# Kernel tuning notes

Hardware: AMD Instinct MI355X
Metric: run time of the kernel (lower is better)

The kernel has to match this reference:

```python
import jax, jax.numpy as jnp
import numpy as np

NEG_SLOPE = 0.2  # PyG GATConv default leaky_relu slope


def _add_self_loops(edge_index, num_nodes):
    loop = jnp.arange(num_nodes, dtype=edge_index.dtype)
    return jnp.concatenate([edge_index, jnp.stack([loop, loop])], axis=1)


def _gat_conv(x, edge_index, W, a_src, a_dst, b, heads, out_c):
    # x: [N, Fin]; W: [Fin, heads*out_c]; a_src/a_dst: [heads, out_c]; b: [heads*out_c]
    N = x.shape[0]
    h = (x @ W).reshape(N, heads, out_c)                       # [N,H,C]
    src, dst = edge_index[0], edge_index[1]
    alpha_src = jnp.einsum('nhc,hc->nh', h, a_src)             # [N,H]
    alpha_dst = jnp.einsum('nhc,hc->nh', h, a_dst)             # [N,H]
    e = jax.nn.leaky_relu(alpha_src[src] + alpha_dst[dst], NEG_SLOPE)  # [E,H]
    # segment softmax over edges grouped by destination node
    m = jax.ops.segment_max(e, dst, num_segments=N)
    m = jnp.where(jnp.isfinite(m), m, jnp.zeros_like(m))
    ex = jnp.exp(e - m[dst])
    denom = jax.ops.segment_sum(ex, dst, num_segments=N)
    alpha = ex / (denom[dst] + 1e-16)                          # [E,H]
    out = jax.ops.segment_sum(h[src] * alpha[:, :, None], dst, num_segments=N)
    return out.reshape(N, heads * out_c) + b


def setup_inputs() -> dict:
    key = jax.random.key(0)
    ks = jax.random.split(key, 16)
    N, E, FIN, HID, HEADS, OUT = 50000, 800000, 128, 32, 4, 64
    x = jax.random.normal(ks[0], (N, FIN), dtype=jnp.float32)
    edge_index = jax.random.randint(ks[1], (2, E), 0, N, dtype=jnp.int64)
    s = 0.1
    inp = {
        'x': x, 'edge_index': edge_index,
        'W0': jax.random.normal(ks[2], (FIN, HEADS * HID), jnp.float32) * s,
        'asrc0': jax.random.normal(ks[3], (HEADS, HID), jnp.float32) * s,
        'adst0': jax.random.normal(ks[4], (HEADS, HID), jnp.float32) * s,
        'b0': jnp.zeros((HEADS * HID,), jnp.float32),
        'W1': jax.random.normal(ks[5], (HEADS * HID, HEADS * HID), jnp.float32) * s,
        'asrc1': jax.random.normal(ks[6], (HEADS, HID), jnp.float32) * s,
        'adst1': jax.random.normal(ks[7], (HEADS, HID), jnp.float32) * s,
        'b1': jnp.zeros((HEADS * HID,), jnp.float32),
        'W2': jax.random.normal(ks[8], (HEADS * HID, OUT), jnp.float32) * s,
        'asrc2': jax.random.normal(ks[9], (1, OUT), jnp.float32) * s,
        'adst2': jax.random.normal(ks[10], (1, OUT), jnp.float32) * s,
        'b2': jnp.zeros((OUT,), jnp.float32),
    }
    return inp


def reference(x, edge_index, W0, asrc0, adst0, b0, W1, asrc1, adst1, b1, W2, asrc2, adst2, b2):
    # Dropout is identity in eval mode.
    N = x.shape[0]
    ei = _add_self_loops(edge_index, N)
    h = _gat_conv(x, ei, W0, asrc0, adst0, b0, heads=4, out_c=32)
    h = jax.nn.relu(h)
    h = _gat_conv(h, ei, W1, asrc1, adst1, b1, heads=4, out_c=32)
    h = jax.nn.relu(h)
    out = _gat_conv(h, ei, W2, asrc2, adst2, b2, heads=1, out_c=64)
    return out
```

## Files before the change

### kernel.cpp

```cpp
#include <hip/hip_runtime.h>


#define NEG_SLOPE 0.2f

typedef _Float16 f16;
typedef f16 f16x8 __attribute__((ext_vector_type(8)));
typedef f16 f16x4 __attribute__((ext_vector_type(4)));
typedef f16 f16x2 __attribute__((ext_vector_type(2)));
typedef float f32x4 __attribute__((ext_vector_type(4)));

__device__ __forceinline__ float lrelu(float v) { return v > 0.f ? v : NEG_SLOPE * v; }


__global__ void fill_zero_kernel(int* __restrict__ p, int n) {
    int i = blockIdx.x * blockDim.x + threadIdx.x;
    if (i < n) p[i] = 0;
}

__global__ __launch_bounds__(256) void bucket_count_kernel(const int* __restrict__ dst, int E,
                                                           int* __restrict__ bcount) {
    __shared__ int lh[256];
    lh[threadIdx.x] = 0;
    __syncthreads();
    int stride = gridDim.x * 256 * 4;
    for (int i = (blockIdx.x * 256 + threadIdx.x) * 4; i < E; i += stride) {
        int4 d = *(const int4*)&dst[i];
        atomicAdd(&lh[d.x >> 8], 1);
        atomicAdd(&lh[d.y >> 8], 1);
        atomicAdd(&lh[d.z >> 8], 1);
        atomicAdd(&lh[d.w >> 8], 1);
    }
    __syncthreads();
    int v = lh[threadIdx.x];
    if (v > 0) atomicAdd(&bcount[threadIdx.x], v);
}

__global__ __launch_bounds__(256) void bucket_scan_kernel(const int* __restrict__ bcount, int NBK,
                                                          int* __restrict__ bbase,
                                                          int* __restrict__ bcursor,
                                                          int* __restrict__ offsets, int N) {
    int t = threadIdx.x;
    int own = (t < NBK) ? bcount[t] : 0;
    int v = own;
    int lane = t & 63, wid = t >> 6;
#pragma unroll
    for (int off = 1; off < 64; off <<= 1) {
        int u = __shfl_up(v, off);
        if (lane >= off) v += u;
    }
    __shared__ int ws[4];
    if (lane == 63) ws[wid] = v;
    __syncthreads();
    int add = 0;
    for (int w = 0; w < wid; ++w) add += ws[w];
    v += add;
    int exc = v - own;
    if (t < NBK) {
        bbase[t] = exc;
        bcursor[t] = exc;
    }
    if (t == 255) {
        bbase[NBK] = v;
        offsets[N] = v;
    }
}

#define SC_TILE 4096
__global__ __launch_bounds__(256) void bucket_scatter_kernel(const int* __restrict__ src,
                                                             const int* __restrict__ dst, int E,
                                                             int* __restrict__ bcursor,
                                                             unsigned int* __restrict__ staging) {
    __shared__ int lh[256];
    __shared__ int lcur[256];
    int tid = threadIdx.x;
    lh[tid] = 0;
    __syncthreads();
    int base = blockIdx.x * SC_TILE + tid * 16;
    int sv[16], dv[16];
    bool act = base < E;
    if (act) {
#pragma unroll
        for (int q = 0; q < 4; ++q) {
            *(int4*)&sv[q * 4] = *(const int4*)&src[base + q * 4];
            *(int4*)&dv[q * 4] = *(const int4*)&dst[base + q * 4];
        }
#pragma unroll
        for (int j = 0; j < 16; ++j) atomicAdd(&lh[dv[j] >> 8], 1);
    }
    __syncthreads();
    int c = lh[tid];
    if (c > 0) lcur[tid] = atomicAdd(&bcursor[tid], c);
    __syncthreads();
    if (act) {
#pragma unroll
        for (int j = 0; j < 16; ++j) {
            int b = dv[j] >> 8;
            int pos = atomicAdd(&lcur[b], 1);
            staging[pos] = (unsigned int)sv[j] | ((unsigned int)(dv[j] & 255) << 16);
        }
    }
}

#define SORT_CAP 8192
__global__ __launch_bounds__(256) void bucket_sort_kernel(const unsigned int* __restrict__ staging,
                                                          const int* __restrict__ bbase,
                                                          int* __restrict__ offsets,
                                                          int* __restrict__ ssrc, int N) {
    __shared__ unsigned int buf[SORT_CAP];
    __shared__ unsigned short sout[SORT_CAP];
    __shared__ int lh[256];
    __shared__ int ws[4];
    int b = blockIdx.x;
    int tid = threadIdx.x;
    int s = bbase[b], e = bbase[b + 1];
    int cnt = e - s;
    lh[tid] = 0;
    __syncthreads();
    bool fits = cnt <= SORT_CAP;
    if (fits) {
        for (int i = tid; i < cnt; i += 256) {
            unsigned int rec = staging[s + i];
            buf[i] = rec;
            atomicAdd(&lh[rec >> 16], 1);
        }
    } else {
        for (int i = tid; i < cnt; i += 256) atomicAdd(&lh[staging[s + i] >> 16], 1);
    }
    __syncthreads();
    int own = lh[tid];
    int v = own;
    int lane = tid & 63, wid = tid >> 6;
#pragma unroll
    for (int off = 1; off < 64; off <<= 1) {
        int u = __shfl_up(v, off);
        if (lane >= off) v += u;
    }
    if (lane == 63) ws[wid] = v;
    __syncthreads();
    int add = 0;
    for (int w = 0; w < wid; ++w) add += ws[w];
    int exc = v + add - own;
    int dstn = (b << 8) + tid;
    if (dstn < N) offsets[dstn] = s + exc;
    __syncthreads();
    lh[tid] = exc;
    __syncthreads();
    if (fits) {
        for (int i = tid; i < cnt; i += 256) {
            unsigned int rec = buf[i];
            int r = atomicAdd(&lh[rec >> 16], 1);
            sout[r] = (unsigned short)(rec & 0xFFFFu);
        }
        __syncthreads();
        for (int i = tid; i < cnt; i += 256) ssrc[s + i] = (int)sout[i];
    } else {
        for (int i = tid; i < cnt; i += 256) {
            unsigned int rec = staging[s + i];
            int r = atomicAdd(&lh[rec >> 16], 1);
            ssrc[s + r] = (int)(rec & 0xFFFFu);
        }
    }
}


__global__ void split_x_kernel(const float* __restrict__ x, f16* __restrict__ xh,
                               f16* __restrict__ xl, int total4) {
    int i = blockIdx.x * blockDim.x + threadIdx.x;
    if (i >= total4) return;
    float4 v = *(const float4*)&x[(size_t)i * 4];
    float vv[4] = {v.x, v.y, v.z, v.w};
    f16x4 h, l;
#pragma unroll
    for (int j = 0; j < 4; ++j) {
        f16 hj = (f16)vv[j];
        h[j] = hj;
        l[j] = (f16)(vv[j] - (float)hj);
    }
    *(f16x4*)&xh[(size_t)i * 4] = h;
    *(f16x4*)&xl[(size_t)i * 4] = l;
}

__global__ void split_w_kernel(const float* __restrict__ W0, const float* __restrict__ W1,
                               const float* __restrict__ W2, f16* __restrict__ w0h,
                               f16* __restrict__ w0l, f16* __restrict__ w1h,
                               f16* __restrict__ w1l, f16* __restrict__ w2h,
                               f16* __restrict__ w2l) {
    int idx = blockIdx.x * 256 + threadIdx.x;
    if (idx < 16384) {
        int k = idx >> 7, c = idx & 127;
        float v = W0[k * 128 + c];
        f16 h = (f16)v;
        w0h[c * 128 + k] = h;
        w0l[c * 128 + k] = (f16)(v - (float)h);
    } else if (idx < 32768) {
        int t = idx - 16384;
        int k = t >> 7, c = t & 127;
        float v = W1[k * 128 + c];
        f16 h = (f16)v;
        w1h[c * 128 + k] = h;
        w1l[c * 128 + k] = (f16)(v - (float)h);
    } else if (idx < 40960) {
        int t = idx - 32768;
        int k = t >> 6, c = t & 63;
        float v = W2[k * 64 + c];
        f16 h = (f16)v;
        w2h[c * 128 + k] = h;
        w2l[c * 128 + k] = (f16)(v - (float)h);
    }
}

template <int FOUT>
__global__ __launch_bounds__(256) void gemm_mfma_kernel(
    const f16* __restrict__ Ah, const f16* __restrict__ Al, const f16* __restrict__ Bh,
    const f16* __restrict__ Bl, f16* __restrict__ H16, int N) {
    constexpr int CT = FOUT / 16;
    __shared__ f16 lw[2][FOUT][72];
    int tid = threadIdx.x;
    int w = tid >> 6, lane = tid & 63;
    int quad = lane >> 4, m = lane & 15;
    int row0 = blockIdx.x * 64 + w * 16;
    int arow = row0 + m;
    if (arow >= N) arow = N - 1;
    const f16* aph = &Ah[(size_t)arow * 128 + quad * 8];
    const f16* apl = &Al[(size_t)arow * 128 + quad * 8];

    f32x4 acc[CT];
#pragma unroll
    for (int t = 0; t < CT; ++t) acc[t] = (f32x4){0.f, 0.f, 0.f, 0.f};

    for (int kh = 0; kh < 2; ++kh) {
        __syncthreads();
        for (int f = tid; f < FOUT * 8; f += 256) {
            int col = f >> 3, ch = f & 7;
            *(f16x8*)&lw[0][col][ch * 8] = *(const f16x8*)&Bh[(size_t)col * 128 + kh * 64 + ch * 8];
            *(f16x8*)&lw[1][col][ch * 8] = *(const f16x8*)&Bl[(size_t)col * 128 + kh * 64 + ch * 8];
        }
        __syncthreads();
#pragma unroll
        for (int kc = 0; kc < 2; ++kc) {
            f16x8 fah = *(const f16x8*)&aph[kh * 64 + kc * 32];
            f16x8 fal = *(const f16x8*)&apl[kh * 64 + kc * 32];
#pragma unroll
            for (int t = 0; t < CT; ++t) {
                f16x8 fbh = *(const f16x8*)&lw[0][t * 16 + m][kc * 32 + quad * 8];
                f16x8 fbl = *(const f16x8*)&lw[1][t * 16 + m][kc * 32 + quad * 8];
                acc[t] = __builtin_amdgcn_mfma_f32_16x16x32_f16(fah, fbh, acc[t], 0, 0, 0);
                acc[t] = __builtin_amdgcn_mfma_f32_16x16x32_f16(fal, fbh, acc[t], 0, 0, 0);
                acc[t] = __builtin_amdgcn_mfma_f32_16x16x32_f16(fah, fbl, acc[t], 0, 0, 0);
            }
        }
    }
#pragma unroll
    for (int r = 0; r < 4; ++r) {
        int row = row0 + quad * 4 + r;
        if (row < N) {
#pragma unroll
            for (int t = 0; t < CT; ++t)
                H16[(size_t)row * FOUT + t * 16 + m] = (f16)acc[t][r];
        }
    }
}

template <int H_, int C>
__global__ void alpha_kernel(const f16* __restrict__ h16, const float* __restrict__ a_src,
                             const float* __restrict__ a_dst, float* __restrict__ asrc,
                             float* __restrict__ adst, int N) {
    int idx = blockIdx.x * blockDim.x + threadIdx.x;
    if (idx >= N * H_) return;
    int n = idx / H_, h = idx % H_;
    const f16* hp = &h16[(size_t)n * H_ * C + h * C];
    const float* as = &a_src[h * C];
    const float* ad = &a_dst[h * C];
    float s1 = 0.f, s2 = 0.f;
#pragma unroll
    for (int c8 = 0; c8 < C / 8; ++c8) {
        f16x8 v = *(const f16x8*)&hp[c8 * 8];
#pragma unroll
        for (int j = 0; j < 8; ++j) {
            float vv = (float)v[j];
            s1 += vv * as[c8 * 8 + j];
            s2 += vv * ad[c8 * 8 + j];
        }
    }
    asrc[idx] = s1;
    adst[idx] = s2;
}

template <int H_, int C, bool RELU, bool SPLIT_OUT>
__global__ __launch_bounds__(256) void aggr_kernel(
    const f16* __restrict__ h16, const float* __restrict__ asrc,
    const float* __restrict__ adst, const float* __restrict__ bias,
    const int* __restrict__ offsets, const int* __restrict__ ssrc, float* __restrict__ outf,
    f16* __restrict__ outh, f16* __restrict__ outl, int N) {
    constexpr int FOUT = H_ * C;
    constexpr int PER = FOUT / 64;
    int wid = threadIdx.x >> 6;
    int lane = threadIdx.x & 63;
    int n = blockIdx.x * 4 + wid;
    if (n >= N) return;
    int c0 = lane * PER;
    int head = c0 / C;

    float adst_h = adst[n * H_ + head];
    float m = lrelu(asrc[n * H_ + head] + adst_h);
    float D = 1.f;
    float S0, S1 = 0.f;
    if (PER == 2) {
        f16x2 hv = *(const f16x2*)&h16[(size_t)n * FOUT + c0];
        S0 = (float)hv[0];
        S1 = (float)hv[1];
    } else {
        S0 = (float)h16[(size_t)n * FOUT + c0];
    }

    int k = offsets[n];
    const int e1 = offsets[n + 1];

    for (; k + 4 <= e1; k += 4) {
        int s0 = ssrc[k], s1 = ssrc[k + 1], s2 = ssrc[k + 2], s3 = ssrc[k + 3];
        f16x2 h0, h1, h2, h3;
        float g0 = 0.f, g1 = 0.f, g2 = 0.f, g3 = 0.f;
        if (PER == 2) {
            h0 = *(const f16x2*)&h16[(size_t)s0 * FOUT + c0];
            h1 = *(const f16x2*)&h16[(size_t)s1 * FOUT + c0];
            h2 = *(const f16x2*)&h16[(size_t)s2 * FOUT + c0];
            h3 = *(const f16x2*)&h16[(size_t)s3 * FOUT + c0];
        } else {
            g0 = (float)h16[(size_t)s0 * FOUT + c0];
            g1 = (float)h16[(size_t)s1 * FOUT + c0];
            g2 = (float)h16[(size_t)s2 * FOUT + c0];
            g3 = (float)h16[(size_t)s3 * FOUT + c0];
        }
        float E0 = lrelu(asrc[s0 * H_ + head] + adst_h);
        float E1 = lrelu(asrc[s1 * H_ + head] + adst_h);
        float E2 = lrelu(asrc[s2 * H_ + head] + adst_h);
        float E3 = lrelu(asrc[s3 * H_ + head] + adst_h);
        float mn = fmaxf(m, fmaxf(fmaxf(E0, E1), fmaxf(E2, E3)));
        float sc = __expf(m - mn);
        m = mn;
        D *= sc;
        S0 *= sc;
        if (PER == 2) S1 *= sc;
        float x0 = __expf(E0 - m), x1 = __expf(E1 - m);
        float x2 = __expf(E2 - m), x3 = __expf(E3 - m);
        D += (x0 + x1) + (x2 + x3);
        if (PER == 2) {
            S0 += x0 * (float)h0[0] + x1 * (float)h1[0] + x2 * (float)h2[0] + x3 * (float)h3[0];
            S1 += x0 * (float)h0[1] + x1 * (float)h1[1] + x2 * (float)h2[1] + x3 * (float)h3[1];
        } else {
            S0 += x0 * g0 + x1 * g1 + x2 * g2 + x3 * g3;
        }
    }
    for (; k < e1; ++k) {
        int s = ssrc[k];
        f16x2 hv;
        float gv = 0.f;
        if (PER == 2) {
            hv = *(const f16x2*)&h16[(size_t)s * FOUT + c0];
        } else {
            gv = (float)h16[(size_t)s * FOUT + c0];
        }
        float E = lrelu(asrc[s * H_ + head] + adst_h);
        float mn = fmaxf(m, E);
        float sc = __expf(m - mn);
        m = mn;
        D *= sc;
        S0 *= sc;
        if (PER == 2) S1 *= sc;
        float ex = __expf(E - m);
        D += ex;
        if (PER == 2) {
            S0 += ex * (float)hv[0];
            S1 += ex * (float)hv[1];
        } else {
            S0 += ex * gv;
        }
    }

    float inv = 1.f / (D + 1e-16f);
    float v0 = S0 * inv + bias[c0];
    if (RELU) v0 = fmaxf(v0, 0.f);
    if (SPLIT_OUT) {
        float v1 = S1 * inv + bias[c0 + 1];
        if (RELU) v1 = fmaxf(v1, 0.f);
        f16 h0 = (f16)v0, h1 = (f16)v1;
        f16x2 hh = {h0, h1};
        f16x2 ll = {(f16)(v0 - (float)h0), (f16)(v1 - (float)h1)};
        *(f16x2*)&outh[(size_t)n * FOUT + c0] = hh;
        *(f16x2*)&outl[(size_t)n * FOUT + c0] = ll;
    } else if (PER == 2) {
        float v1 = S1 * inv + bias[c0 + 1];
        if (RELU) v1 = fmaxf(v1, 0.f);
        *(float2*)&outf[(size_t)n * FOUT + c0] = make_float2(v0, v1);
    } else {
        outf[(size_t)n * FOUT + c0] = v0;
    }
}

extern "C" void kernel_launch(void* const* d_in, const int* in_sizes, int n_in,
                              void* d_out, int out_size, void* d_ws, size_t ws_size,
                              hipStream_t stream) {
    const float* x = (const float*)d_in[0];
    const int* ei = (const int*)d_in[1];
    const float* W0 = (const float*)d_in[2];
    const float* as0 = (const float*)d_in[3];
    const float* ad0 = (const float*)d_in[4];
    const float* b0 = (const float*)d_in[5];
    const float* W1 = (const float*)d_in[6];
    const float* as1 = (const float*)d_in[7];
    const float* ad1 = (const float*)d_in[8];
    const float* b1 = (const float*)d_in[9];
    const float* W2 = (const float*)d_in[10];
    const float* as2 = (const float*)d_in[11];
    const float* ad2 = (const float*)d_in[12];
    const float* b2 = (const float*)d_in[13];

    const int N = in_sizes[0] / 128;
    const int E = in_sizes[1] / 2;
    const int NBK = (N + 255) >> 8;

    float* aS = (float*)d_ws;
    float* aD = aS + (size_t)N * 4;
    f16* h16 = (f16*)(aD + (size_t)N * 4);
    f16* xh = h16 + (size_t)N * 128;
    f16* xl = xh + (size_t)N * 128;
    f16* w0h = xl + (size_t)N * 128;
    f16* w0l = w0h + 16384;
    f16* w1h = w0l + 16384;
    f16* w1l = w1h + 16384;
    f16* w2h = w1l + 16384;
    f16* w2l = w2h + 8192;
    int* offsets = (int*)(w2l + 8192);
    int* ssrc = offsets + N + 1;
    unsigned int* staging = (unsigned int*)(ssrc + E);
    int* bcount = (int*)(staging + E);
    int* bbase = bcount + NBK;
    int* bcursor = bbase + NBK + 1;

    fill_zero_kernel<<<1, 256, 0, stream>>>(bcount, NBK);
    bucket_count_kernel<<<196, 256, 0, stream>>>(ei + E, E, bcount);
    bucket_scan_kernel<<<1, 256, 0, stream>>>(bcount, NBK, bbase, bcursor, offsets, N);
    bucket_scatter_kernel<<<(E + SC_TILE - 1) / SC_TILE, 256, 0, stream>>>(ei, ei + E, E, bcursor,
                                                                           staging);
    bucket_sort_kernel<<<NBK, 256, 0, stream>>>(staging, bbase, offsets, ssrc, N);

    split_x_kernel<<<(N * 32 + 255) / 256, 256, 0, stream>>>(x, xh, xl, N * 32);
    split_w_kernel<<<160, 256, 0, stream>>>(W0, W1, W2, w0h, w0l, w1h, w1l, w2h, w2l);

    const int gGemm = (N + 63) / 64;
    const int gAggr = (N + 3) / 4;

    gemm_mfma_kernel<128><<<gGemm, 256, 0, stream>>>(xh, xl, w0h, w0l, h16, N);
    alpha_kernel<4, 32><<<(N * 4 + 255) / 256, 256, 0, stream>>>(h16, as0, ad0, aS, aD, N);
    aggr_kernel<4, 32, true, true><<<gAggr, 256, 0, stream>>>(h16, aS, aD, b0, offsets, ssrc,
                                                              nullptr, xh, xl, N);
    gemm_mfma_kernel<128><<<gGemm, 256, 0, stream>>>(xh, xl, w1h, w1l, h16, N);
    alpha_kernel<4, 32><<<(N * 4 + 255) / 256, 256, 0, stream>>>(h16, as1, ad1, aS, aD, N);
    aggr_kernel<4, 32, true, true><<<gAggr, 256, 0, stream>>>(h16, aS, aD, b1, offsets, ssrc,
                                                              nullptr, xh, xl, N);
    gemm_mfma_kernel<64><<<gGemm, 256, 0, stream>>>(xh, xl, w2h, w2l, h16, N);
    alpha_kernel<1, 64><<<(N + 255) / 256, 256, 0, stream>>>(h16, as2, ad2, aS, aD, N);
    aggr_kernel<1, 64, false, false><<<gAggr, 256, 0, stream>>>(h16, aS, aD, b2, offsets, ssrc,
                                                                (float*)d_out, nullptr, nullptr, N);
}
```

Before: 322.6 us.

## Precompute per-edge softmax weights using the self-loop logit as stabilizer

Adds an edge-weight kernel that computes exp(e - e_self) per edge and head, using each destination's self-loop logit in place of the running maximum. The aggregation kernel then reads these precomputed weights with vector loads instead of gathering attention scores and doing online-max rescaling and exp for every lane. To make this possible, the sort kernel now packs the destination index into the upper 16 bits of each sorted source entry and drops its shared-memory staging, which gives up coalesced writes. In exchange it adds an extra E×heads float buffer written and read per layer, adds a launch per layer, and risks exp overflow if an edge logit far exceeds the self-loop logit.

```diff
diff --git a/kernel.cpp b/kernel.cpp
--- a/kernel.cpp
+++ b/kernel.cpp
@@ -101,13 +101,10 @@
     }
 }
 
-#define SORT_CAP 8192
 __global__ __launch_bounds__(256) void bucket_sort_kernel(const unsigned int* __restrict__ staging,
                                                           const int* __restrict__ bbase,
                                                           int* __restrict__ offsets,
                                                           int* __restrict__ ssrc, int N) {
-    __shared__ unsigned int buf[SORT_CAP];
-    __shared__ unsigned short sout[SORT_CAP];
     __shared__ int lh[256];
     __shared__ int ws[4];
     int b = blockIdx.x;
@@ -116,16 +113,7 @@
     int cnt = e - s;
     lh[tid] = 0;
     __syncthreads();
-    bool fits = cnt <= SORT_CAP;
-    if (fits) {
-        for (int i = tid; i < cnt; i += 256) {
-            unsigned int rec = staging[s + i];
-            buf[i] = rec;
-            atomicAdd(&lh[rec >> 16], 1);
-        }
-    } else {
-        for (int i = tid; i < cnt; i += 256) atomicAdd(&lh[staging[s + i] >> 16], 1);
-    }
+    for (int i = tid; i < cnt; i += 256) atomicAdd(&lh[staging[s + i] >> 16], 1);
     __syncthreads();
     int own = lh[tid];
     int v = own;
@@ -145,20 +133,12 @@
     __syncthreads();
     lh[tid] = exc;
     __syncthreads();
-    if (fits) {
-        for (int i = tid; i < cnt; i += 256) {
-            unsigned int rec = buf[i];
-            int r = atomicAdd(&lh[rec >> 16], 1);
-            sout[r] = (unsigned short)(rec & 0xFFFFu);
-        }
-        __syncthreads();
-        for (int i = tid; i < cnt; i += 256) ssrc[s + i] = (int)sout[i];
-    } else {
-        for (int i = tid; i < cnt; i += 256) {
-            unsigned int rec = staging[s + i];
-            int r = atomicAdd(&lh[rec >> 16], 1);
-            ssrc[s + r] = (int)(rec & 0xFFFFu);
-        }
+    for (int i = tid; i < cnt; i += 256) {
+        unsigned int rec = staging[s + i];
+        int dlow = rec >> 16;
+        int r = atomicAdd(&lh[dlow], 1);
+        unsigned int full = (rec & 0xFFFFu) | ((unsigned int)((b << 8) | dlow) << 16);
+        ssrc[s + r] = (int)full;
     }
 }
 
@@ -286,12 +266,32 @@
     adst[idx] = s2;
 }
 
+template <int H_>
+__global__ void edgew_kernel(const int* __restrict__ ssrc, const float* __restrict__ asrc,
+                             const float* __restrict__ adst, float* __restrict__ w, int E) {
+    int k = blockIdx.x * 256 + threadIdx.x;
+    if (k >= E) return;
+    unsigned int rec = (unsigned int)ssrc[k];
+    int s = rec & 0xFFFFu, d = rec >> 16;
+    if (H_ == 4) {
+        float4 a_s = *(const float4*)&asrc[s * 4];
+        float4 a_dd = *(const float4*)&adst[d * 4];
+        float4 a_sd = *(const float4*)&asrc[d * 4];
+        w[0 * E + k] = __expf(lrelu(a_s.x + a_dd.x) - lrelu(a_sd.x + a_dd.x));
+        w[1 * E + k] = __expf(lrelu(a_s.y + a_dd.y) - lrelu(a_sd.y + a_dd.y));
+        w[2 * E + k] = __expf(lrelu(a_s.z + a_dd.z) - lrelu(a_sd.z + a_dd.z));
+        w[3 * E + k] = __expf(lrelu(a_s.w + a_dd.w) - lrelu(a_sd.w + a_dd.w));
+    } else {
+        w[k] = __expf(lrelu(asrc[s] + adst[d]) - lrelu(asrc[d] + adst[d]));
+    }
+}
+
 template <int H_, int C, bool RELU, bool SPLIT_OUT>
 __global__ __launch_bounds__(256) void aggr_kernel(
-    const f16* __restrict__ h16, const float* __restrict__ asrc,
-    const float* __restrict__ adst, const float* __restrict__ bias,
-    const int* __restrict__ offsets, const int* __restrict__ ssrc, float* __restrict__ outf,
-    f16* __restrict__ outh, f16* __restrict__ outl, int N) {
+    const f16* __restrict__ h16, const float* __restrict__ wedge,
+    const float* __restrict__ bias, const int* __restrict__ offsets,
+    const int* __restrict__ ssrc, float* __restrict__ outf, f16* __restrict__ outh,
+    f16* __restrict__ outl, int N, int E) {
     constexpr int FOUT = H_ * C;
     constexpr int PER = FOUT / 64;
     int wid = threadIdx.x >> 6;
@@ -300,80 +300,66 @@
     if (n >= N) return;
     int c0 = lane * PER;
     int head = c0 / C;
-
-    float adst_h = adst[n * H_ + head];
-    float m = lrelu(asrc[n * H_ + head] + adst_h);
+    const float* wb = wedge + head * E;
+
     float D = 1.f;
     float S0, S1 = 0.f;
     if (PER == 2) {
-        f16x2 hv = *(const f16x2*)&h16[(size_t)n * FOUT + c0];
+        f16x2 hv = *(const f16x2*)&h16[n * FOUT + c0];
         S0 = (float)hv[0];
         S1 = (float)hv[1];
     } else {
-        S0 = (float)h16[(size_t)n * FOUT + c0];
+        S0 = (float)h16[n * FOUT + c0];
     }
 
     int k = offsets[n];
     const int e1 = offsets[n + 1];
 
+    for (; k < e1 && (k & 3); ++k) {
+        int s = ssrc[k] & 0xFFFF;
+        float w = wb[k];
+        D += w;
+        if (PER == 2) {
+            f16x2 hv = *(const f16x2*)&h16[s * FOUT + c0];
+            S0 += w * (float)hv[0];
+            S1 += w * (float)hv[1];
+        } else {
+            S0 += w * (float)h16[s * FOUT + c0];
+        }
+    }
     for (; k + 4 <= e1; k += 4) {
-        int s0 = ssrc[k], s1 = ssrc[k + 1], s2 = ssrc[k + 2], s3 = ssrc[k + 3];
-        f16x2 h0, h1, h2, h3;
-        float g0 = 0.f, g1 = 0.f, g2 = 0.f, g3 = 0.f;
+        int4 pk = *(const int4*)&ssrc[k];
+        float4 wv = *(const float4*)&wb[k];
+        int s0 = pk.x & 0xFFFF, s1 = pk.y & 0xFFFF, s2 = pk.z & 0xFFFF, s3 = pk.w & 0xFFFF;
         if (PER == 2) {
-            h0 = *(const f16x2*)&h16[(size_t)s0 * FOUT + c0];
-            h1 = *(const f16x2*)&h16[(size_t)s1 * FOUT + c0];
-            h2 = *(const f16x2*)&h16[(size_t)s2 * FOUT + c0];
-            h3 = *(const f16x2*)&h16[(size_t)s3 * FOUT + c0];
+            f16x2 h0 = *(const f16x2*)&h16[s0 * FOUT + c0];
+            f16x2 h1 = *(const f16x2*)&h16[s1 * FOUT + c0];
+            f16x2 h2 = *(const f16x2*)&h16[s2 * FOUT + c0];
+            f16x2 h3 = *(const f16x2*)&h16[s3 * FOUT + c0];
+            D += (wv.x + wv.y) + (wv.z + wv.w);
+            S0 += wv.x * (float)h0[0] + wv.y * (float)h1[0] + wv.z * (float)h2[0] +
+                  wv.w * (float)h3[0];
+            S1 += wv.x * (float)h0[1] + wv.y * (float)h1[1] + wv.z * (float)h2[1] +
+                  wv.w * (float)h3[1];
         } else {
-            g0 = (float)h16[(size_t)s0 * FOUT + c0];
-            g1 = (float)h16[(size_t)s1 * FOUT + c0];
-            g2 = (float)h16[(size_t)s2 * FOUT + c0];
-            g3 = (float)h16[(size_t)s3 * FOUT + c0];
-        }
-        float E0 = lrelu(asrc[s0 * H_ + head] + adst_h);
-        float E1 = lrelu(asrc[s1 * H_ + head] + adst_h);
-        float E2 = lrelu(asrc[s2 * H_ + head] + adst_h);
-        float E3 = lrelu(asrc[s3 * H_ + head] + adst_h);
-        float mn = fmaxf(m, fmaxf(fmaxf(E0, E1), fmaxf(E2, E3)));
-        float sc = __expf(m - mn);
-        m = mn;
-        D *= sc;
-        S0 *= sc;
-        if (PER == 2) S1 *= sc;
-        float x0 = __expf(E0 - m), x1 = __expf(E1 - m);
-        float x2 = __expf(E2 - m), x3 = __expf(E3 - m);
-        D += (x0 + x1) + (x2 + x3);
+            float g0 = (float)h16[s0 * FOUT + c0];
+            float g1 = (float)h16[s1 * FOUT + c0];
+            float g2 = (float)h16[s2 * FOUT + c0];
+            float g3 = (float)h16[s3 * FOUT + c0];
+            D += (wv.x + wv.y) + (wv.z + wv.w);
+            S0 += wv.x * g0 + wv.y * g1 + wv.z * g2 + wv.w * g3;
+        }
+    }
+    for (; k < e1; ++k) {
+        int s = ssrc[k] & 0xFFFF;
+        float w = wb[k];
+        D += w;
         if (PER == 2) {
-            S0 += x0 * (float)h0[0] + x1 * (float)h1[0] + x2 * (float)h2[0] + x3 * (float)h3[0];
-            S1 += x0 * (float)h0[1] + x1 * (float)h1[1] + x2 * (float)h2[1] + x3 * (float)h3[1];
+            f16x2 hv = *(const f16x2*)&h16[s * FOUT + c0];
+            S0 += w * (float)hv[0];
+            S1 += w * (float)hv[1];
         } else {
-            S0 += x0 * g0 + x1 * g1 + x2 * g2 + x3 * g3;
-        }
-    }
-    for (; k < e1; ++k) {
-        int s = ssrc[k];
-        f16x2 hv;
-        float gv = 0.f;
-        if (PER == 2) {
-            hv = *(const f16x2*)&h16[(size_t)s * FOUT + c0];
-        } else {
-            gv = (float)h16[(size_t)s * FOUT + c0];
-        }
-        float E = lrelu(asrc[s * H_ + head] + adst_h);
-        float mn = fmaxf(m, E);
-        float sc = __expf(m - mn);
-        m = mn;
-        D *= sc;
-        S0 *= sc;
-        if (PER == 2) S1 *= sc;
-        float ex = __expf(E - m);
-        D += ex;
-        if (PER == 2) {
-            S0 += ex * (float)hv[0];
-            S1 += ex * (float)hv[1];
-        } else {
-            S0 += ex * gv;
+            S0 += w * (float)h16[s * FOUT + c0];
         }
     }
 
@@ -386,14 +372,14 @@
         f16 h0 = (f16)v0, h1 = (f16)v1;
         f16x2 hh = {h0, h1};
         f16x2 ll = {(f16)(v0 - (float)h0), (f16)(v1 - (float)h1)};
-        *(f16x2*)&outh[(size_t)n * FOUT + c0] = hh;
-        *(f16x2*)&outl[(size_t)n * FOUT + c0] = ll;
+        *(f16x2*)&outh[n * FOUT + c0] = hh;
+        *(f16x2*)&outl[n * FOUT + c0] = ll;
     } else if (PER == 2) {
         float v1 = S1 * inv + bias[c0 + 1];
         if (RELU) v1 = fmaxf(v1, 0.f);
-        *(float2*)&outf[(size_t)n * FOUT + c0] = make_float2(v0, v1);
+        *(float2*)&outf[n * FOUT + c0] = make_float2(v0, v1);
     } else {
-        outf[(size_t)n * FOUT + c0] = v0;
+        outf[n * FOUT + c0] = v0;
     }
 }
 
@@ -433,7 +419,8 @@
     int* offsets = (int*)(w2l + 8192);
     int* ssrc = offsets + N + 1;
     unsigned int* staging = (unsigned int*)(ssrc + E);
-    int* bcount = (int*)(staging + E);
+    float* wedge = (float*)(staging + E);
+    int* bcount = (int*)(wedge + (size_t)E * 4);
     int* bbase = bcount + NBK;
     int* bcursor = bbase + NBK + 1;
 
@@ -449,17 +436,22 @@
 
     const int gGemm = (N + 63) / 64;
     const int gAggr = (N + 3) / 4;
+    const int gE = (E + 255) / 256;
 
     gemm_mfma_kernel<128><<<gGemm, 256, 0, stream>>>(xh, xl, w0h, w0l, h16, N);
     alpha_kernel<4, 32><<<(N * 4 + 255) / 256, 256, 0, stream>>>(h16, as0, ad0, aS, aD, N);
-    aggr_kernel<4, 32, true, true><<<gAggr, 256, 0, stream>>>(h16, aS, aD, b0, offsets, ssrc,
-                                                              nullptr, xh, xl, N);
+    edgew_kernel<4><<<gE, 256, 0, stream>>>(ssrc, aS, aD, wedge, E);
+    aggr_kernel<4, 32, true, true><<<gAggr, 256, 0, stream>>>(h16, wedge, b0, offsets, ssrc,
+                                                              nullptr, xh, xl, N, E);
     gemm_mfma_kernel<128><<<gGemm, 256, 0, stream>>>(xh, xl, w1h, w1l, h16, N);
     alpha_kernel<4, 32><<<(N * 4 + 255) / 256, 256, 0, stream>>>(h16, as1, ad1, aS, aD, N);
-    aggr_kernel<4, 32, true, true><<<gAggr, 256, 0, stream>>>(h16, aS, aD, b1, offsets, ssrc,
-                                                              nullptr, xh, xl, N);
+    edgew_kernel<4><<<gE, 256, 0, stream>>>(ssrc, aS, aD, wedge, E);
+    aggr_kernel<4, 32, true, true><<<gAggr, 256, 0, stream>>>(h16, wedge, b1, offsets, ssrc,
+                                                              nullptr, xh, xl, N, E);
     gemm_mfma_kernel<64><<<gGemm, 256, 0, stream>>>(xh, xl, w2h, w2l, h16, N);
     alpha_kernel<1, 64><<<(N + 255) / 256, 256, 0, stream>>>(h16, as2, ad2, aS, aD, N);
-    aggr_kernel<1, 64, false, false><<<gAggr, 256, 0, stream>>>(h16, aS, aD, b2, offsets, ssrc,
-                                                                (float*)d_out, nullptr, nullptr, N);
-}
+    edgew_kernel<1><<<gE, 256, 0, stream>>>(ssrc, aS, aD, wedge, E);
+    aggr_kernel<1, 64, false, false><<<gAggr, 256, 0, stream>>>(h16, wedge, b2, offsets, ssrc,
+                                                                (float*)d_out, nullptr, nullptr,
+                                                                N, E);
+}
```

Measured after the change: 348.7 us. 1.08x slower.
